# Optimization experiments

Hardware: AMD Instinct MI355X
Metric: run time of the kernel (lower is better)

The kernel has to match this reference:

```python
import jax, jax.numpy as jnp
from jax import lax
import numpy as np


def conv2d(x, w, pad):
    # x: NCHW, w: OIHW
    return lax.conv_general_dilated(x, w, (1, 1), [(pad, pad), (pad, pad)],
                                    dimension_numbers=("NCHW", "OIHW", "NCHW"))


def make_dct_dict(num_atoms, num_dims):
    i = np.arange(num_atoms)[:, None].astype(np.float64)
    n = np.arange(num_dims)[None, :].astype(np.float64)
    w = np.cos((2.0 * n + 1.0) * i * (np.pi / (2.0 * num_dims)))
    w = w / np.linalg.norm(w, axis=1, keepdims=True)
    return jnp.asarray(w.T, dtype=jnp.float32)  # [num_dims, num_atoms]


def setup_inputs() -> dict:
    key = jax.random.key(0)
    B, C, H, W = 8, 64, 64, 64      # C = num_dims
    A = 256                          # num_atoms
    ks = jax.random.split(key, 10)
    s = 0.05
    Dict = make_dct_dict(A, C)       # [C, A]
    L = jnp.sum(Dict ** 2)           # ||Dict||_F^2 (scalar parameter)
    return {
        "x": jax.random.normal(ks[0], (B, C, H, W), jnp.float32),
        "conv_w": jax.random.normal(ks[1], (A, C, 3, 3), jnp.float32) * s,
        "conv_b": jax.random.normal(ks[2], (A,), jnp.float32) * s,
        "res1_w1": jax.random.normal(ks[3], (A // 2, A, 3, 3), jnp.float32) * s,
        "res1_w2": jax.random.normal(ks[4], (A, A // 2, 1, 1), jnp.float32) * s,
        "res2_w1": jax.random.normal(ks[5], (A // 2, A, 3, 3), jnp.float32) * s,
        "res2_w2": jax.random.normal(ks[6], (A, A // 2, 1, 1), jnp.float32) * s,
        "ca_w1": jax.random.normal(ks[7], (A // 16, A), jnp.float32) * s,  # Linear(A, A//16)
        "ca_w2": jax.random.normal(ks[8], (A, A // 16), jnp.float32) * s,  # Linear(A//16, A)
        "sa_w": jax.random.normal(ks[9], (1, 2, 3, 3), jnp.float32) * s,
        "Dict": Dict,
        "L": L,
        "num_iters": 16,
    }


def reference(x, conv_w, conv_b, res1_w1, res1_w2, res2_w1, res2_w2,
              ca_w1, ca_w2, sa_w, Dict, L, num_iters):
    def res_block(h, w1, w2):
        t = conv2d(jax.nn.relu(h), w1, 1)
        t = conv2d(jax.nn.relu(t), w2, 0)
        return h + t

    l = conv2d(x, conv_w, 1) + conv_b[None, :, None, None]
    l = res_block(l, res1_w1, res1_w2)
    l = res_block(l, res2_w1, res2_w2)

    # CBAM: channel attention (shared MLP on avg/max pooled features)
    avg = jnp.mean(l, axis=(2, 3))  # [B, A]
    mx = jnp.max(l, axis=(2, 3))
    fc = lambda v: jax.nn.relu(v @ ca_w1.T) @ ca_w2.T
    l = l * jax.nn.sigmoid(fc(avg) + fc(mx))[:, :, None, None]
    # CBAM: spatial attention
    s2 = jnp.concatenate([jnp.mean(l, axis=1, keepdims=True),
                          jnp.max(l, axis=1, keepdims=True)], axis=1)  # [B,2,H,W]
    l = l * jax.nn.sigmoid(conv2d(s2, sa_w, 1))

    lam = jnp.transpose(l / L, (0, 2, 3, 1))   # [B,H,W,A] per-position thresholds
    xp = jnp.transpose(x, (0, 2, 3, 1))        # [B,H,W,C]

    A = Dict.shape[1]
    S = (jnp.eye(A, dtype=Dict.dtype) - (Dict.T @ Dict) / L).T  # [A,A]
    y = xp @ Dict                               # [B,H,W,A]
    yL = y / L

    soft = lambda v: jnp.sign(v) * jnp.maximum(jnp.abs(v) - lam, 0.0)

    z0 = soft(y)

    def step(z, _):
        return soft(z @ S + yL), None

    z, _ = lax.scan(step, z0, None, length=num_iters)
    x_recon = z @ Dict.T                        # [B,H,W,C]

    return (jnp.transpose(z, (0, 3, 1, 2)),
            jnp.transpose(x_recon, (0, 3, 1, 2)),
            Dict)
```

## Files before the change

### kernel.cpp

```cpp
#include <hip/hip_runtime.h>
#include <hip/hip_bf16.h>

typedef __attribute__((ext_vector_type(8))) short short8v;
typedef __attribute__((ext_vector_type(4))) short short4v;
typedef __attribute__((ext_vector_type(4))) float float4v;

__device__ __forceinline__ unsigned short f2bu(float v){
  __hip_bfloat16 h = __float2bfloat16(v);
  union { __hip_bfloat16 h; unsigned short u; } cv; cv.h = h; return cv.u;
}

__device__ __forceinline__ float softt(float v, float lam){
  float t = fmaxf(fabsf(v) - lam, 0.f);
  float r = copysignf(t, v);
  return (v == 0.f) ? 0.f : r;
}

__global__ void k_Lin(const float* __restrict__ Lsrc, float* __restrict__ Lb){
  Lb[0] = Lsrc[0];
}

__global__ void k_gram(const float* __restrict__ D, unsigned short* __restrict__ Gb){
  int j = blockIdx.x, a = threadIdx.x;
  float acc = 0.f;
  for (int c = 0; c < 64; ++c)
    acc += D[c*256 + j] * D[c*256 + a];
  Gb[j*256 + a] = f2bu(acc);
}

__global__ void k_transpD(const float* __restrict__ D, float* __restrict__ DT,
                          unsigned short* __restrict__ DTb){
  int gid = blockIdx.x * 256 + threadIdx.x;
  if (gid < 16384) {
    int a = gid >> 6, c = gid & 63;
    float v = D[c*256 + a];
    DT[gid] = v;
    DTb[gid] = f2bu(v);
  }
}

__global__ void k_castw(const float* __restrict__ w, unsigned short* __restrict__ wb,
                        int n){
  int gid = blockIdx.x * 256 + threadIdx.x;
  if (gid < n) wb[gid] = f2bu(w[gid]);
}

__global__ void k_permw3(const float* __restrict__ w, unsigned short* __restrict__ wb,
                         int logI, int n){
  int gid = blockIdx.x * 256 + threadIdx.x;
  if (gid >= n) return;
  int I = 1 << logI;
  int i = gid & (I - 1);
  int t = gid >> logI;
  int o = t / 9;
  int r = t - o * 9;
  wb[gid] = f2bu(w[((o << logI) + i) * 9 + r]);
}

template<int KS, int CIN, bool BIAS, bool RES, bool WF32, bool WBF>
__global__ __launch_bounds__(256) void k_conv(
    const unsigned short* __restrict__ in, const unsigned short* __restrict__ wb,
    const float* __restrict__ bias, const float* res, float* outf,
    unsigned short* __restrict__ outb, int Cout)
{
  constexpr int NCH  = CIN / 32;
  constexpr int LNCH = (NCH == 2) ? 1 : (NCH == 4 ? 2 : 3);
  constexpr int K    = KS * KS * CIN;

  __shared__ unsigned short Asb[64][40];
  __shared__ unsigned short Bsb[128][40];

  const int tid = threadIdx.x;
  int bx = blockIdx.x;
  { const int cpx = gridDim.x >> 3; bx = (bx & 7) * cpx + (bx >> 3); }
  const int m0  = bx * 64;
  const int n0  = blockIdx.y * 128;
  const int b   = m0 >> 12;
  const int hw0 = m0 & 4095;
  const int h   = hw0 >> 6;
  const int w0  = hw0 & 63;

  const int sm  = tid & 63;
  const int sq8 = tid >> 6;
  const int bn  = tid & 127;
  const int bq  = tid >> 7;

  const int w   = tid >> 6;
  const int ln  = tid & 63;
  const int q   = ln >> 4;
  const int l16 = ln & 15;

  float4v acc[2][4];
  #pragma unroll
  for (int nt = 0; nt < 2; ++nt)
    #pragma unroll
    for (int mt = 0; mt < 4; ++mt)
      acc[nt][mt] = (float4v){0.f, 0.f, 0.f, 0.f};

  int sA = 0, sB = NCH;
  if (KS == 3) { sA = (h == 0 ? 3 : 0) * NCH; sB = (h == 63 ? 6 : 9) * NCH; }

  short8v a_r;
  short8v b_r0, b_r1;

  auto pref = [&](int s){
    const int r    = s >> LNCH;
    const int ccid = s & (NCH - 1);
    int hh = h, ww = w0 + sm;
    bool ok = true;
    if (KS == 3) {
      const int r3 = r / 3;
      const int dw = r - r3 * 3 - 1;
      hh = h + r3 - 1;
      ww += dw;
      ok = ((unsigned)ww < 64u);
    }
    a_r = (short8v){0,0,0,0,0,0,0,0};
    if (ok) {
      const unsigned short* ap = in +
          (((size_t)(b * CIN + ccid * 32 + sq8 * 8)) << 12) + (hh << 6) + ww;
      #pragma unroll
      for (int j = 0; j < 8; ++j)
        a_r[j] = (short)ap[(size_t)j << 12];
    }
    const unsigned short* bp = wb + (size_t)(n0 + bn) * K + s * 32 + bq * 16;
    b_r0 = *(const short8v*)(bp);
    b_r1 = *(const short8v*)(bp + 8);
  };

  pref(sA);
  for (int s = sA; s < sB; ) {
    *(short8v*)(&Asb[sm][sq8 * 8])      = a_r;
    *(short8v*)(&Bsb[bn][bq * 16])      = b_r0;
    *(short8v*)(&Bsb[bn][bq * 16 + 8])  = b_r1;
    __syncthreads();
    const int sn = s + 1;
    if (sn < sB) pref(sn);
    short8v Af[4];
    #pragma unroll
    for (int mt = 0; mt < 4; ++mt)
      Af[mt] = *(const short8v*)(&Asb[mt * 16 + l16][q * 8]);
    #pragma unroll
    for (int nt = 0; nt < 2; ++nt) {
      short8v Bf = *(const short8v*)(&Bsb[w * 32 + nt * 16 + l16][q * 8]);
      #pragma unroll
      for (int mt = 0; mt < 4; ++mt)
        acc[nt][mt] = __builtin_amdgcn_mfma_f32_16x16x32_bf16(
            Af[mt], Bf, acc[nt][mt], 0, 0, 0);
    }
    __syncthreads();
    s = sn;
  }

  #pragma unroll
  for (int nt = 0; nt < 2; ++nt) {
    const int n = n0 + w * 32 + nt * 16 + l16;
    float bv = 0.f;
    if (BIAS) bv = bias[n];
    #pragma unroll
    for (int mt = 0; mt < 4; ++mt) {
      const size_t base = (((size_t)(b * Cout + n)) << 12) + hw0 + mt * 16 + q * 4;
      float o[4];
      #pragma unroll
      for (int r2 = 0; r2 < 4; ++r2) o[r2] = acc[nt][mt][r2] + bv;
      if (RES) {
        float4 r4 = *(const float4*)(res + base);
        o[0] += r4.x; o[1] += r4.y; o[2] += r4.z; o[3] += r4.w;
      }
      if (WF32) {
        float4 o4; o4.x = o[0]; o4.y = o[1]; o4.z = o[2]; o4.w = o[3];
        *(float4*)(outf + base) = o4;
      }
      if (WBF) {
        short4v s4;
        #pragma unroll
        for (int r2 = 0; r2 < 4; ++r2) s4[r2] = (short)f2bu(fmaxf(o[r2], 0.f));
        *(short4v*)(outb + base) = s4;
      }
    }
  }
}

__global__ void k_pool(const float* __restrict__ l, float* __restrict__ avg,
                       float* __restrict__ mx){
  int b = blockIdx.y, a = blockIdx.x, tid = threadIdx.x;
  const float* p = l + ((size_t)(b * 256 + a) << 12);
  float s = 0.f, m = -1e30f;
  for (int i = tid; i < 4096; i += 256) { float v = p[i]; s += v; m = fmaxf(m, v); }
  __shared__ float ss[256], sm[256];
  ss[tid] = s; sm[tid] = m; __syncthreads();
  for (int o = 128; o > 0; o >>= 1) {
    if (tid < o) { ss[tid] += ss[tid+o]; sm[tid] = fmaxf(sm[tid], sm[tid+o]); }
    __syncthreads();
  }
  if (tid == 0) { avg[b*256+a] = ss[0] * (1.f/4096.f); mx[b*256+a] = sm[0]; }
}

__global__ void k_ca(const float* __restrict__ avg, const float* __restrict__ mx,
                     const float* __restrict__ w1, const float* __restrict__ w2,
                     float* __restrict__ cscale){
  int b = blockIdx.x, tid = threadIdx.x;
  __shared__ float h[16];
  if (tid < 16) {
    float sa = 0.f, sm = 0.f;
    for (int a = 0; a < 256; ++a) {
      float w = w1[tid*256 + a];
      sa += avg[b*256 + a] * w;
      sm += mx[b*256 + a] * w;
    }
    h[tid] = fmaxf(sa, 0.f) + fmaxf(sm, 0.f);
  }
  __syncthreads();
  float s = 0.f;
  for (int j = 0; j < 16; ++j) s += h[j] * w2[tid*16 + j];
  cscale[b*256 + tid] = 1.f / (1.f + __expf(-s));
}

__global__ void k_s2(const float* __restrict__ l, const float* __restrict__ cscale,
                     float* __restrict__ s2){
  int b = blockIdx.y;
  int hw = blockIdx.x * 256 + threadIdx.x;
  const float* p  = l + (((size_t)b * 256) << 12) + hw;
  const float* cs = cscale + b * 256;
  float s = 0.f, m = -1e30f;
  for (int a = 0; a < 256; ++a) {
    float v = p[(size_t)a << 12] * cs[a];
    s += v; m = fmaxf(m, v);
  }
  s2[((b*2) << 12) + hw]   = s * (1.f/256.f);
  s2[((b*2+1) << 12) + hw] = m;
}

__global__ void k_sa(const float* __restrict__ s2, const float* __restrict__ w,
                     float* __restrict__ sa){
  int b = blockIdx.y;
  int hw = blockIdx.x * 256 + threadIdx.x;
  int h = hw >> 6, ww = hw & 63;
  float acc = 0.f;
  for (int ch = 0; ch < 2; ++ch)
    for (int dh = -1; dh <= 1; ++dh)
      for (int dw = -1; dw <= 1; ++dw) {
        int hh = h + dh, wc = ww + dw;
        if ((unsigned)hh < 64u && (unsigned)wc < 64u)
          acc += s2[((b*2+ch) << 12) + (hh << 6) + wc] * w[ch*9 + (dh+1)*3 + (dw+1)];
      }
  sa[(b << 12) + hw] = 1.f / (1.f + __expf(-acc));
}

#define ZSTR 272
#define XTS 80

__global__ __launch_bounds__(1024, 4) void k_lista(
    const unsigned short* __restrict__ xb,
    const unsigned short* __restrict__ DTb,
    const unsigned short* __restrict__ Gb,
    const float* __restrict__ lmap, const float* __restrict__ csc,
    const float* __restrict__ sav, const float* __restrict__ Lb,
    float* __restrict__ zout)
{
  __shared__ unsigned short zbuf[2][32 * ZSTR];

  const int tid = threadIdx.x;
  const int m0  = blockIdx.x * 32;
  const int b   = m0 >> 12;
  const int hw0 = m0 & 4095;
  const float invL = 1.0f / Lb[0];

  unsigned short* xTb = &zbuf[1][0];
  {
    const int i  = tid & 31;
    const int c0 = tid >> 5;
    xTb[i * XTS + c0]      = xb[((b * 64 + c0) << 12) + hw0 + i];
    xTb[i * XTS + c0 + 32] = xb[((b * 64 + c0 + 32) << 12) + hw0 + i];
  }

  const int w   = tid >> 6;
  const int ln  = tid & 63;
  const int q   = ln >> 4;
  const int l16 = ln & 15;

  short8v Sg[8];
  #pragma unroll
  for (int ks = 0; ks < 8; ++ks)
    Sg[ks] = *(const short8v*)(
        Gb + (size_t)(w * 16 + l16) * 256 + ks * 32 + q * 8);

  __syncthreads();

  float z[2][4], yl[2][4], lamr[2][4];

  {
    const short8v A0 = *(const short8v*)(DTb + (w*16 + l16) * 64 + q * 8);
    const short8v A1 = *(const short8v*)(DTb + (w*16 + l16) * 64 + 32 + q * 8);
    #pragma unroll
    for (int pt = 0; pt < 2; ++pt) {
      float4v a = {0.f, 0.f, 0.f, 0.f};
      const short8v B0 = *(const short8v*)(&xTb[(pt*16 + l16) * XTS + q * 8]);
      const short8v B1 = *(const short8v*)(&xTb[(pt*16 + l16) * XTS + 32 + q * 8]);
      a = __builtin_amdgcn_mfma_f32_16x16x32_bf16(A0, B0, a, 0, 0, 0);
      a = __builtin_amdgcn_mfma_f32_16x16x32_bf16(A1, B1, a, 0, 0, 0);
      const int p = pt * 16 + l16;
      short4v pk;
      #pragma unroll
      for (int r = 0; r < 4; ++r) {
        const int atom = w * 16 + q * 4 + r;
        const float lv = lmap[(((size_t)(b * 256 + atom)) << 12) + hw0 + p];
        const float sv = sav[(b << 12) + hw0 + p];
        const float cv = csc[b * 256 + atom];
        const float lm = ((lv * cv) * sv) * invL;
        const float yv = a[r];
        lamr[pt][r] = lm;
        yl[pt][r]   = yv * invL;
        const float z0 = softt(yv, lm);
        z[pt][r] = z0;
        pk[r] = (short)f2bu(z0);
      }
      *(short4v*)(&zbuf[0][p * ZSTR + w * 16 + q * 4]) = pk;
    }
  }

  #pragma unroll
  for (int ks = 0; ks < 8; ++ks)
    asm volatile("" : "+v"(Sg[ks]));

  __syncthreads();

  int cur = 0;
  for (int it = 0; it < 16; ++it) {
    float4v acc[2];
    acc[0] = (float4v){0.f, 0.f, 0.f, 0.f};
    acc[1] = (float4v){0.f, 0.f, 0.f, 0.f};

    #pragma unroll
    for (int pt = 0; pt < 2; ++pt) {
      const unsigned short* zrow = &zbuf[cur][(pt * 16 + l16) * ZSTR + q * 8];
      #pragma unroll
      for (int ks = 0; ks < 8; ++ks) {
        const short8v B = *(const short8v*)(zrow + ks * 32);
        acc[pt] = __builtin_amdgcn_mfma_f32_16x16x32_bf16(Sg[ks], B, acc[pt], 0, 0, 0);
      }
    }
    #pragma unroll
    for (int pt = 0; pt < 2; ++pt) {
      const int p = pt * 16 + l16;
      short4v pk;
      #pragma unroll
      for (int r = 0; r < 4; ++r) {
        const float u  = fmaf(-invL, acc[pt][r], z[pt][r] + yl[pt][r]);
        const float nz = softt(u, lamr[pt][r]);
        z[pt][r] = nz;
        pk[r] = (short)f2bu(nz);
      }
      *(short4v*)(&zbuf[cur ^ 1][p * ZSTR + w * 16 + q * 4]) = pk;
    }
    __syncthreads();
    cur ^= 1;
  }

  #pragma unroll
  for (int pt = 0; pt < 2; ++pt) {
    const int p = pt * 16 + l16;
    float4 o;
    o.x = z[pt][0]; o.y = z[pt][1]; o.z = z[pt][2]; o.w = z[pt][3];
    *(float4*)(&zout[(size_t)(m0 + p) * 256 + w * 16 + q * 4]) = o;
  }
}

__global__ __launch_bounds__(256) void k_recon_simple(
    const float* __restrict__ z, const float* __restrict__ DT,
    float* __restrict__ out1)
{
  __shared__ float zs[16][256];
  const int tid = threadIdx.x;
  const int r0  = blockIdx.x * 16;
  const int b   = r0 >> 12;
  const int hw0 = r0 & 4095;

  for (int idx = tid; idx < 4096; idx += 256) {
    int r = idx >> 8, k = idx & 255;
    zs[r][k] = z[(r0 + r) * 256 + k];
  }
  __syncthreads();

  const int c  = tid & 63;
  const int rg = tid >> 6;
  float acc[4] = {0.f, 0.f, 0.f, 0.f};
  for (int a = 0; a < 256; ++a) {
    float d = DT[a * 64 + c];
    #pragma unroll
    for (int i = 0; i < 4; ++i) acc[i] += zs[rg + 4*i][a] * d;
  }
  #pragma unroll
  for (int i = 0; i < 4; ++i) {
    int r = rg + 4*i;
    out1[((b * 64 + c) << 12) + hw0 + r] = acc[i];
  }
}

__global__ __launch_bounds__(256) void k_zout_t(const float* __restrict__ z,
                                                float* __restrict__ out0){
  __shared__ float zs[64][65];
  const int tid = threadIdx.x;
  const int hwt = blockIdx.x * 64;
  const int at  = blockIdx.y * 64;
  const int b   = blockIdx.z;
  const int j   = tid & 63;
  const int i0  = tid >> 6;
  #pragma unroll
  for (int k = 0; k < 16; ++k) {
    int i = i0 + k * 4;
    zs[i][j] = z[(size_t)(b * 4096 + hwt + i) * 256 + at + j];
  }
  __syncthreads();
  #pragma unroll
  for (int k = 0; k < 16; ++k) {
    int i = i0 + k * 4;
    out0[(((size_t)(b * 256 + at + i)) << 12) + hwt + j] = zs[j][i];
  }
}

__global__ void k_dictout_f32(const float* __restrict__ D, float* __restrict__ out2){
  int i = blockIdx.x * 256 + threadIdx.x;
  if (i < 16384) out2[i] = D[i];
}

extern "C" void kernel_launch(void* const* d_in, const int* in_sizes, int n_in,
                              void* d_out, int out_size, void* d_ws, size_t ws_size,
                              hipStream_t stream)
{
  (void)in_sizes; (void)n_in; (void)out_size; (void)ws_size;

  const float* x    = (const float*)d_in[0];
  const float* cw   = (const float*)d_in[1];
  const float* cb   = (const float*)d_in[2];
  const float* r1w1 = (const float*)d_in[3];
  const float* r1w2 = (const float*)d_in[4];
  const float* r2w1 = (const float*)d_in[5];
  const float* r2w2 = (const float*)d_in[6];
  const float* caw1 = (const float*)d_in[7];
  const float* caw2 = (const float*)d_in[8];
  const float* saw  = (const float*)d_in[9];
  const float* D    = (const float*)d_in[10];
  const float* Lsrc = (const float*)d_in[11];

  float* p = (float*)d_ws;
  float* DT   = p; p += 16384;
  float* Lb   = p; p += 8;
  unsigned short* Gb  = (unsigned short*)p; p += 32768;
  unsigned short* DTb = (unsigned short*)p; p += 8192;
  unsigned short* cwb   = (unsigned short*)p; p += 73728;
  unsigned short* r1w1b = (unsigned short*)p; p += 147456;
  unsigned short* r1w2b = (unsigned short*)p; p += 16384;
  unsigned short* r2w1b = (unsigned short*)p; p += 147456;
  unsigned short* r2w2b = (unsigned short*)p; p += 16384;
  float* avg  = p; p += 2048;
  float* mx   = p; p += 2048;
  float* csc  = p; p += 2048;
  float* s2   = p; p += 65536;
  float* sa   = p; p += 32768;
  float* l    = p; p += 8388608;
  float* scr  = p; p += 8388608;
  float* zt   = p; p += 8388608;
  float* z    = zt;

  unsigned short* xb = (unsigned short*)scr;
  unsigned short* lb = (unsigned short*)(scr + 1048576);
  unsigned short* tb = (unsigned short*)(scr + 1048576 + 4194304);

  float* out0 = (float*)d_out;
  float* out1 = out0 + (size_t)8*256*4096;
  float* out2 = out1 + (size_t)8*64*4096;

  dim3 b256(256);

  k_Lin<<<dim3(1), dim3(1), 0, stream>>>(Lsrc, Lb);
  k_gram<<<dim3(256), b256, 0, stream>>>(D, Gb);
  k_transpD<<<dim3(64), b256, 0, stream>>>(D, DT, DTb);
  k_permw3<<<dim3(576),  b256, 0, stream>>>(cw,   cwb,   6, 147456);
  k_permw3<<<dim3(1152), b256, 0, stream>>>(r1w1, r1w1b, 8, 294912);
  k_castw <<<dim3(128),  b256, 0, stream>>>(r1w2, r1w2b, 32768);
  k_permw3<<<dim3(1152), b256, 0, stream>>>(r2w1, r2w1b, 8, 294912);
  k_castw <<<dim3(128),  b256, 0, stream>>>(r2w2, r2w2b, 32768);
  k_castw <<<dim3(8192), b256, 0, stream>>>(x, xb, 2097152);

  k_conv<3,  64, true,  false, true,  true ><<<dim3(512, 2), b256, 0, stream>>>(
      xb, cwb, cb, (const float*)nullptr, l, lb, 256);
  k_conv<3, 256, false, false, false, true ><<<dim3(512, 1), b256, 0, stream>>>(
      lb, r1w1b, (const float*)nullptr, (const float*)nullptr, (float*)nullptr, tb, 128);
  k_conv<1, 128, false, true,  true,  true ><<<dim3(512, 2), b256, 0, stream>>>(
      tb, r1w2b, (const float*)nullptr, l, l, lb, 256);
  k_conv<3, 256, false, false, false, true ><<<dim3(512, 1), b256, 0, stream>>>(
      lb, r2w1b, (const float*)nullptr, (const float*)nullptr, (float*)nullptr, tb, 128);
  k_conv<1, 128, false, true,  true,  false><<<dim3(512, 2), b256, 0, stream>>>(
      tb, r2w2b, (const float*)nullptr, l, l, (unsigned short*)nullptr, 256);

  k_pool<<<dim3(256, 8), b256, 0, stream>>>(l, avg, mx);
  k_ca<<<dim3(8), b256, 0, stream>>>(avg, mx, caw1, caw2, csc);
  k_s2<<<dim3(16, 8), b256, 0, stream>>>(l, csc, s2);
  k_sa<<<dim3(16, 8), b256, 0, stream>>>(s2, saw, sa);

  k_lista<<<dim3(1024), dim3(1024), 0, stream>>>(xb, DTb, Gb, l, csc, sa, Lb, z);

  k_recon_simple<<<dim3(2048), b256, 0, stream>>>(z, DT, out1);
  k_zout_t<<<dim3(64, 4, 8), b256, 0, stream>>>(z, out0);
  k_dictout_f32<<<dim3(64), b256, 0, stream>>>(D, out2);
}
```

Measured before the change: 492.4 us.

## Retile LISTA kernel to 256-thread blocks of 16 positions with swizzled LDS

The LISTA iteration kernel moves from 1024-thread blocks over 32 positions to 256-thread blocks over 16 positions. Each wave now holds 64 rows of the S matrix in registers (four 16-row tiles) and reuses each loaded z fragment across four MFMAs. The padded z buffer is replaced by an XOR-swizzled layout to avoid LDS bank conflicts. Smaller blocks should make the per-iteration barrier cheaper and cut LDS reads per MFMA, but each thread holds four times as many S registers, which raises register pressure and may lower occupancy.

```diff
diff --git a/kernel.cpp b/kernel.cpp
--- a/kernel.cpp
+++ b/kernel.cpp
@@ -247,10 +247,13 @@
   sa[(b << 12) + hw] = 1.f / (1.f + __expf(-acc));
 }
 
-#define ZSTR 272
 #define XTS 80
 
-__global__ __launch_bounds__(1024, 4) void k_lista(
+__device__ __forceinline__ int zoff(int pos, int au8){
+  return pos * 256 + (((au8 ^ (pos & 15)) & 31) << 3);
+}
+
+__global__ __launch_bounds__(256, 2) void k_lista(
     const unsigned short* __restrict__ xb,
     const unsigned short* __restrict__ DTb,
     const unsigned short* __restrict__ Gb,
@@ -258,20 +261,23 @@
     const float* __restrict__ sav, const float* __restrict__ Lb,
     float* __restrict__ zout)
 {
-  __shared__ unsigned short zbuf[2][32 * ZSTR];
+  __shared__ unsigned short zbuf[2][16 * 256];
 
   const int tid = threadIdx.x;
-  const int m0  = blockIdx.x * 32;
+  const int m0  = blockIdx.x * 16;
   const int b   = m0 >> 12;
   const int hw0 = m0 & 4095;
   const float invL = 1.0f / Lb[0];
 
   unsigned short* xTb = &zbuf[1][0];
   {
-    const int i  = tid & 31;
-    const int c0 = tid >> 5;
-    xTb[i * XTS + c0]      = xb[((b * 64 + c0) << 12) + hw0 + i];
-    xTb[i * XTS + c0 + 32] = xb[((b * 64 + c0 + 32) << 12) + hw0 + i];
+    const int i  = tid & 15;
+    const int c0 = tid >> 4;
+    #pragma unroll
+    for (int cc = 0; cc < 4; ++cc) {
+      int c = c0 + cc * 16;
+      xTb[i * XTS + c] = xb[((b * 64 + c) << 12) + hw0 + i];
+    }
   }
 
   const int w   = tid >> 6;
@@ -279,90 +285,92 @@
   const int q   = ln >> 4;
   const int l16 = ln & 15;
 
-  short8v Sg[8];
-  #pragma unroll
-  for (int ks = 0; ks < 8; ++ks)
-    Sg[ks] = *(const short8v*)(
-        Gb + (size_t)(w * 16 + l16) * 256 + ks * 32 + q * 8);
+  short8v Sg[4][8];
+  #pragma unroll
+  for (int at = 0; at < 4; ++at)
+    #pragma unroll
+    for (int ks = 0; ks < 8; ++ks)
+      Sg[at][ks] = *(const short8v*)(
+          Gb + (size_t)(w * 64 + at * 16 + l16) * 256 + ks * 32 + q * 8);
 
   __syncthreads();
 
-  float z[2][4], yl[2][4], lamr[2][4];
+  float z[4][4], yl[4][4], lamr[4][4];
 
   {
-    const short8v A0 = *(const short8v*)(DTb + (w*16 + l16) * 64 + q * 8);
-    const short8v A1 = *(const short8v*)(DTb + (w*16 + l16) * 64 + 32 + q * 8);
-    #pragma unroll
-    for (int pt = 0; pt < 2; ++pt) {
+    const short8v B0 = *(const short8v*)(&xTb[l16 * XTS + q * 8]);
+    const short8v B1 = *(const short8v*)(&xTb[l16 * XTS + 32 + q * 8]);
+    #pragma unroll
+    for (int at = 0; at < 4; ++at) {
+      const int abase = w * 64 + at * 16;
+      const short8v A0 = *(const short8v*)(DTb + (abase + l16) * 64 + q * 8);
+      const short8v A1 = *(const short8v*)(DTb + (abase + l16) * 64 + 32 + q * 8);
       float4v a = {0.f, 0.f, 0.f, 0.f};
-      const short8v B0 = *(const short8v*)(&xTb[(pt*16 + l16) * XTS + q * 8]);
-      const short8v B1 = *(const short8v*)(&xTb[(pt*16 + l16) * XTS + 32 + q * 8]);
       a = __builtin_amdgcn_mfma_f32_16x16x32_bf16(A0, B0, a, 0, 0, 0);
       a = __builtin_amdgcn_mfma_f32_16x16x32_bf16(A1, B1, a, 0, 0, 0);
-      const int p = pt * 16 + l16;
       short4v pk;
       #pragma unroll
       for (int r = 0; r < 4; ++r) {
-        const int atom = w * 16 + q * 4 + r;
-        const float lv = lmap[(((size_t)(b * 256 + atom)) << 12) + hw0 + p];
-        const float sv = sav[(b << 12) + hw0 + p];
+        const int atom = abase + q * 4 + r;
+        const float lv = lmap[(((size_t)(b * 256 + atom)) << 12) + hw0 + l16];
+        const float sv = sav[(b << 12) + hw0 + l16];
         const float cv = csc[b * 256 + atom];
         const float lm = ((lv * cv) * sv) * invL;
         const float yv = a[r];
-        lamr[pt][r] = lm;
-        yl[pt][r]   = yv * invL;
+        lamr[at][r] = lm;
+        yl[at][r]   = yv * invL;
         const float z0 = softt(yv, lm);
-        z[pt][r] = z0;
+        z[at][r] = z0;
         pk[r] = (short)f2bu(z0);
       }
-      *(short4v*)(&zbuf[0][p * ZSTR + w * 16 + q * 4]) = pk;
-    }
-  }
-
-  #pragma unroll
-  for (int ks = 0; ks < 8; ++ks)
-    asm volatile("" : "+v"(Sg[ks]));
-
+      *(short4v*)(&zbuf[0][zoff(l16, w * 8 + at * 2 + (q >> 1)) + (q & 1) * 4]) = pk;
+    }
+  }
   __syncthreads();
 
   int cur = 0;
   for (int it = 0; it < 16; ++it) {
-    float4v acc[2];
-    acc[0] = (float4v){0.f, 0.f, 0.f, 0.f};
-    acc[1] = (float4v){0.f, 0.f, 0.f, 0.f};
-
-    #pragma unroll
-    for (int pt = 0; pt < 2; ++pt) {
-      const unsigned short* zrow = &zbuf[cur][(pt * 16 + l16) * ZSTR + q * 8];
+    #pragma unroll
+    for (int at = 0; at < 4; ++at)
       #pragma unroll
-      for (int ks = 0; ks < 8; ++ks) {
-        const short8v B = *(const short8v*)(zrow + ks * 32);
-        acc[pt] = __builtin_amdgcn_mfma_f32_16x16x32_bf16(Sg[ks], B, acc[pt], 0, 0, 0);
-      }
-    }
-    #pragma unroll
-    for (int pt = 0; pt < 2; ++pt) {
-      const int p = pt * 16 + l16;
+      for (int ks = 0; ks < 8; ++ks)
+        asm volatile("" : "+v"(Sg[at][ks]));
+
+    float4v acc[4];
+    #pragma unroll
+    for (int at = 0; at < 4; ++at)
+      acc[at] = (float4v){0.f, 0.f, 0.f, 0.f};
+
+    #pragma unroll
+    for (int ks = 0; ks < 8; ++ks) {
+      const short8v B = *(const short8v*)(&zbuf[cur][zoff(l16, ks * 4 + q)]);
+      acc[0] = __builtin_amdgcn_mfma_f32_16x16x32_bf16(Sg[0][ks], B, acc[0], 0, 0, 0);
+      acc[1] = __builtin_amdgcn_mfma_f32_16x16x32_bf16(Sg[1][ks], B, acc[1], 0, 0, 0);
+      acc[2] = __builtin_amdgcn_mfma_f32_16x16x32_bf16(Sg[2][ks], B, acc[2], 0, 0, 0);
+      acc[3] = __builtin_amdgcn_mfma_f32_16x16x32_bf16(Sg[3][ks], B, acc[3], 0, 0, 0);
+    }
+
+    #pragma unroll
+    for (int at = 0; at < 4; ++at) {
       short4v pk;
       #pragma unroll
       for (int r = 0; r < 4; ++r) {
-        const float u  = fmaf(-invL, acc[pt][r], z[pt][r] + yl[pt][r]);
-        const float nz = softt(u, lamr[pt][r]);
-        z[pt][r] = nz;
+        const float u  = fmaf(-invL, acc[at][r], z[at][r] + yl[at][r]);
+        const float nz = softt(u, lamr[at][r]);
+        z[at][r] = nz;
         pk[r] = (short)f2bu(nz);
       }
-      *(short4v*)(&zbuf[cur ^ 1][p * ZSTR + w * 16 + q * 4]) = pk;
+      *(short4v*)(&zbuf[cur ^ 1][zoff(l16, w * 8 + at * 2 + (q >> 1)) + (q & 1) * 4]) = pk;
     }
     __syncthreads();
     cur ^= 1;
   }
 
   #pragma unroll
-  for (int pt = 0; pt < 2; ++pt) {
-    const int p = pt * 16 + l16;
+  for (int at = 0; at < 4; ++at) {
     float4 o;
-    o.x = z[pt][0]; o.y = z[pt][1]; o.z = z[pt][2]; o.w = z[pt][3];
-    *(float4*)(&zout[(size_t)(m0 + p) * 256 + w * 16 + q * 4]) = o;
+    o.x = z[at][0]; o.y = z[at][1]; o.z = z[at][2]; o.w = z[at][3];
+    *(float4*)(&zout[(size_t)(m0 + l16) * 256 + w * 64 + at * 16 + q * 4]) = o;
   }
 }
 
@@ -499,7 +507,7 @@
   k_s2<<<dim3(16, 8), b256, 0, stream>>>(l, csc, s2);
   k_sa<<<dim3(16, 8), b256, 0, stream>>>(s2, saw, sa);
 
-  k_lista<<<dim3(1024), dim3(1024), 0, stream>>>(xb, DTb, Gb, l, csc, sa, Lb, z);
+  k_lista<<<dim3(2048), b256, 0, stream>>>(xb, DTb, Gb, l, csc, sa, Lb, z);
 
   k_recon_simple<<<dim3(2048), b256, 0, stream>>>(z, DT, out1);
   k_zout_t<<<dim3(64, 4, 8), b256, 0, stream>>>(z, out0);
```

After: 479.0 us. 2.7% less time.
